# Performance work log

Measured on AMD Instinct MI355X. Metric: run time of the kernel, lower is better.

The kernel has to match this reference:

```python
import jax, jax.numpy as jnp
import numpy as np

B, L, HID, NH, HD = 2, 2048, 512, 8, 64
FACTOR = 5
SAMPLE_K = 40  # min(factor * ceil(ln(L)), L)
N_TOP = 40     # min(factor * ceil(ln(L)), L)


def setup_inputs() -> dict:
    key = jax.random.key(0)
    ks = jax.random.split(key, 10)
    s = 1.0 / np.sqrt(HID).astype(np.float32)
    return {
        "hidden_states": jax.random.normal(ks[0], (B, L, HID), jnp.float32),
        "index_sample": jax.random.randint(ks[1], (L, SAMPLE_K), 0, L, jnp.int32),
        "Wq": jax.random.normal(ks[2], (HID, HID), jnp.float32) * s,
        "bq": jnp.zeros((HID,), jnp.float32),
        "Wk": jax.random.normal(ks[3], (HID, HID), jnp.float32) * s,
        "bk": jnp.zeros((HID,), jnp.float32),
        "Wv": jax.random.normal(ks[4], (HID, HID), jnp.float32) * s,
        "bv": jnp.zeros((HID,), jnp.float32),
        "Wo": jax.random.normal(ks[5], (HID, HID), jnp.float32) * s,
        "bo": jnp.zeros((HID,), jnp.float32),
    }


def _heads(x):
    # [B, L, HID] -> [B, NH, L, HD]
    return x.reshape(B, L, NH, HD).transpose(0, 2, 1, 3)


def reference(hidden_states, index_sample, Wq, bq, Wk, bk, Wv, bv, Wo, bo):
    # projections (torch Linear: x @ W.T + b)
    q = _heads(hidden_states @ Wq.T + bq)  # [B,NH,L,HD]
    k = _heads(hidden_states @ Wk.T + bk)
    v = _heads(hidden_states @ Wv.T + bv)

    # --- prob QK: random key sampling per query position ---
    # gather sampled keys: [B,NH,L,SAMPLE_K,HD]
    k_samp = k[:, :, index_sample, :]
    qk_samp = jnp.einsum('bhld,bhlsd->bhls', q, k_samp)
    # sparsity measure M(q) = max - mean (mean uses full k_len as in source)
    m = qk_samp.max(axis=-1) - qk_samp.sum(axis=-1) / L  # [B,NH,L]
    _, m_top = jax.lax.top_k(m, N_TOP)  # [B,NH,N_TOP]

    # selected queries -> dense scores against all keys
    q_red = jnp.take_along_axis(q, m_top[..., None], axis=2)  # [B,NH,N_TOP,HD]
    scores = jnp.einsum('bhqd,bhkd->bhqk', q_red, k) / np.sqrt(HD).astype(np.float32)

    # --- context: mean(V) baseline, scatter attended rows (no mask, eval dropout) ---
    attn = jax.nn.softmax(scores, axis=-1)  # [B,NH,N_TOP,L]
    ctx_sel = jnp.einsum('bhqk,bhkd->bhqd', attn, v)  # [B,NH,N_TOP,HD]
    context = jnp.broadcast_to(v.mean(axis=2, keepdims=True), (B, NH, L, HD))
    bi = jnp.arange(B)[:, None, None]
    hi = jnp.arange(NH)[None, :, None]
    context = context.at[bi, hi, m_top].set(ctx_sel)  # [B,NH,L,HD]

    out = context.transpose(0, 2, 1, 3).reshape(B, L, HID) @ Wo.T + bo
    return out
```

## Files before the change

### kernel.cpp

```cpp
#include <hip/hip_runtime.h>
#include <hip/hip_bf16.h>
#include <math.h>

#define B_   2
#define L_   2048
#define HID_ 512
#define NH_  8
#define HD_  64
#define SK_  40
#define NTOP_ 40
#define NBH_ (B_ * NH_)
#define NROW_ (B_ * L_)
#define CHUNK_ 64
#define NCH_ (L_ / CHUNK_)
#define NTILE_ 64

__global__ __launch_bounds__(256, 2) void proj_kernel(
    const float* __restrict__ A,
    const float* __restrict__ Wq, const float* __restrict__ bq,
    const float* __restrict__ Wk, const float* __restrict__ bk,
    const float* __restrict__ Wv, const float* __restrict__ bv,
    float* __restrict__ qo, float* __restrict__ ko, float* __restrict__ vo,
    float* __restrict__ vmp)
{
    __shared__ __align__(16) float As[32][68];
    __shared__ __align__(16) float Bs[3][32][68];
    __shared__ float red[16][64];

    const float* Ws[3]  = {Wq, Wk, Wv};
    const float* bs3[3] = {bq, bk, bv};
    float*       os3[3] = {qo, ko, vo};

    const int t    = threadIdx.x;
    const int row0 = blockIdx.x * 64;
    const int h    = blockIdx.y;
    const int col0 = h * 64;
    const int ry   = t >> 4;
    const int cx   = t & 15;
    const int a_k4 = t & 7;
    const int sub  = t >> 3;

    float acc[3][4][4] = {};
    float4 pa[2], pb[3][2];

    #pragma unroll
    for (int i = 0; i < 2; ++i)
        pa[i] = *reinterpret_cast<const float4*>(
            &A[(size_t)(row0 + i * 32 + sub) * HID_ + (a_k4 << 2)]);
    #pragma unroll
    for (int w = 0; w < 3; ++w)
        #pragma unroll
        for (int i = 0; i < 2; ++i)
            pb[w][i] = *reinterpret_cast<const float4*>(
                &Ws[w][(size_t)(col0 + i * 32 + sub) * HID_ + (a_k4 << 2)]);

    for (int ks = 0; ks < 16; ++ks) {
        #pragma unroll
        for (int i = 0; i < 2; ++i) {
            const int a_row = i * 32 + sub;
            const int slot = (a_row >> 2) ^ a_k4;
            float* p = &As[a_k4 << 2][slot * 4 + (a_row & 3)];
            p[0 * 68] = pa[i].x; p[1 * 68] = pa[i].y;
            p[2 * 68] = pa[i].z; p[3 * 68] = pa[i].w;
        }
        #pragma unroll
        for (int w = 0; w < 3; ++w)
            #pragma unroll
            for (int i = 0; i < 2; ++i) {
                const int b_col = i * 32 + sub;
                const int slot = (b_col >> 2) ^ a_k4;
                float* p = &Bs[w][a_k4 << 2][slot * 4 + (b_col & 3)];
                p[0 * 68] = pb[w][i].x; p[1 * 68] = pb[w][i].y;
                p[2 * 68] = pb[w][i].z; p[3 * 68] = pb[w][i].w;
            }
        __syncthreads();

        if (ks < 15) {
            const int k0 = (ks + 1) * 32;
            #pragma unroll
            for (int i = 0; i < 2; ++i)
                pa[i] = *reinterpret_cast<const float4*>(
                    &A[(size_t)(row0 + i * 32 + sub) * HID_ + k0 + (a_k4 << 2)]);
            #pragma unroll
            for (int w = 0; w < 3; ++w)
                #pragma unroll
                for (int i = 0; i < 2; ++i)
                    pb[w][i] = *reinterpret_cast<const float4*>(
                        &Ws[w][(size_t)(col0 + i * 32 + sub) * HID_ + k0 + (a_k4 << 2)]);
        }

        #pragma unroll
        for (int kk = 0; kk < 32; ++kk) {
            const int v = kk >> 2;
            const float4 a0 = *reinterpret_cast<const float4*>(
                &As[kk][(ry ^ v) << 2]);
            const float as[4] = {a0.x, a0.y, a0.z, a0.w};
            #pragma unroll
            for (int w = 0; w < 3; ++w) {
                const float4 b0 = *reinterpret_cast<const float4*>(
                    &Bs[w][kk][(cx ^ v) << 2]);
                #pragma unroll
                for (int i = 0; i < 4; ++i) {
                    acc[w][i][0] = fmaf(as[i], b0.x, acc[w][i][0]);
                    acc[w][i][1] = fmaf(as[i], b0.y, acc[w][i][1]);
                    acc[w][i][2] = fmaf(as[i], b0.z, acc[w][i][2]);
                    acc[w][i][3] = fmaf(as[i], b0.w, acc[w][i][3]);
                }
            }
        }
        __syncthreads();
    }

    const int b_ = row0 >> 11;
    float4 bbv;
    #pragma unroll
    for (int w = 0; w < 3; ++w) {
        const float4 bb = *reinterpret_cast<const float4*>(&bs3[w][col0 + (cx << 2)]);
        if (w == 2) bbv = bb;
        #pragma unroll
        for (int i = 0; i < 4; ++i) {
            const int row = row0 + ry * 4 + i;
            const int l   = row & (L_ - 1);
            float4 ob;
            ob.x = acc[w][i][0] + bb.x;
            ob.y = acc[w][i][1] + bb.y;
            ob.z = acc[w][i][2] + bb.z;
            ob.w = acc[w][i][3] + bb.w;
            *reinterpret_cast<float4*>(
                &os3[w][(((size_t)(b_ * NH_ + h)) * L_ + l) * HD_ + (cx << 2)]) = ob;
        }
    }

    #pragma unroll
    for (int j = 0; j < 4; ++j) {
        float s_ = 0.f;
        #pragma unroll
        for (int i = 0; i < 4; ++i) s_ += acc[2][i][j];
        const float bj = (j == 0) ? bbv.x : (j == 1) ? bbv.y : (j == 2) ? bbv.z : bbv.w;
        red[ry][(cx << 2) + j] = s_ + 4.f * bj;
    }
    __syncthreads();
    if (t < 64) {
        float s_ = 0.f;
        #pragma unroll
        for (int r = 0; r < 16; ++r) s_ += red[r][t];
        vmp[((size_t)blockIdx.x * NH_ + h) * HD_ + t] = s_;
    }
}

__global__ __launch_bounds__(512) void base_kernel(
    const float* __restrict__ vmp, const float* __restrict__ Wo,
    const float* __restrict__ bo, float* __restrict__ vmean,
    float* __restrict__ base_out)
{
    const int b = blockIdx.x;
    const int t = threadIdx.x;
    __shared__ float vm[HID_];

    float s = 0.f;
    #pragma unroll
    for (int tl = 0; tl < 32; ++tl)
        s += vmp[((size_t)(b * 32 + tl) * NH_) * HD_ + t];
    const float mv = s * (1.0f / (float)L_);
    vmean[b * HID_ + t] = mv;
    vm[t] = mv;
    __syncthreads();

    float acc = bo[t];
    for (int c = 0; c < HID_; c += 4) {
        float4 w = *reinterpret_cast<const float4*>(&Wo[(size_t)t * HID_ + c]);
        acc = fmaf(vm[c + 0], w.x, acc);
        acc = fmaf(vm[c + 1], w.y, acc);
        acc = fmaf(vm[c + 2], w.z, acc);
        acc = fmaf(vm[c + 3], w.w, acc);
    }
    base_out[b * HID_ + t] = acc;
}

__global__ __launch_bounds__(256) void sample_m_kernel(
    const float* __restrict__ q, const float* __restrict__ k,
    const int* __restrict__ idx, float* __restrict__ m)
{
    const int wid  = blockIdx.x * 4 + (threadIdx.x >> 6);
    const int lane = threadIdx.x & 63;
    const int bh = wid >> 11;
    const int l  = wid & (L_ - 1);
    const int grp = lane >> 4, gl = lane & 15;

    const float4 qf = *reinterpret_cast<const float4*>(&q[(bh * L_ + l) * HD_ + (gl << 2)]);

    float mx = -INFINITY, sm = 0.f;
    #pragma unroll
    for (int it = 0; it < 10; ++it) {
        const int s  = it * 4 + grp;
        const int ki = idx[l * SK_ + s];
        const float4 kf = *reinterpret_cast<const float4*>(&k[(bh * L_ + ki) * HD_ + (gl << 2)]);
        float p = qf.x * kf.x + qf.y * kf.y + qf.z * kf.z + qf.w * kf.w;
        p += __shfl_xor(p, 1);
        p += __shfl_xor(p, 2);
        p += __shfl_xor(p, 4);
        p += __shfl_xor(p, 8);
        mx = fmaxf(mx, p);
        sm += p;
    }
    mx = fmaxf(mx, __shfl_xor(mx, 16));
    mx = fmaxf(mx, __shfl_xor(mx, 32));
    sm += __shfl_xor(sm, 16);
    sm += __shfl_xor(sm, 32);
    if (lane == 0) m[bh * L_ + l] = mx - sm * (1.0f / (float)L_);
}

__global__ __launch_bounds__(256) void topk_kernel(
    const float* __restrict__ m, int* __restrict__ m_top)
{
    const int bh = blockIdx.x;
    const int t  = threadIdx.x;
    const int lane = t & 63, wv = t >> 6;

    unsigned xv[8];
    #pragma unroll
    for (int i = 0; i < 8; ++i) {
        unsigned x = __float_as_uint(m[bh * L_ + i * 256 + t]);
        xv[i] = (x & 0x80000000u) ? ~x : (x | 0x80000000u);
    }

    __shared__ int cnt[2][4];
    __shared__ int s_outcnt, s_tieCnt;
    __shared__ int tie[256];
    if (t == 0) { s_outcnt = 0; s_tieCnt = 0; }

    unsigned pref = 0;
    for (int bit = 31; bit >= 0; --bit) {
        const unsigned test = pref | (1u << bit);
        int c = 0;
        #pragma unroll
        for (int i = 0; i < 8; ++i) c += (xv[i] >= test);
        #pragma unroll
        for (int off = 1; off < 64; off <<= 1) c += __shfl_xor(c, off);
        if (lane == 0) cnt[bit & 1][wv] = c;
        __syncthreads();
        const int tot = cnt[bit & 1][0] + cnt[bit & 1][1]
                      + cnt[bit & 1][2] + cnt[bit & 1][3];
        if (tot >= NTOP_) pref = test;
    }
    const unsigned V = pref;

    #pragma unroll
    for (int i = 0; i < 8; ++i) {
        const unsigned x = xv[i];
        const int idxv = i * 256 + t;
        if (x > V) {
            const int p = atomicAdd(&s_outcnt, 1);
            m_top[bh * NTOP_ + p] = idxv;
        } else if (x == V) {
            const int p = atomicAdd(&s_tieCnt, 1);
            if (p < 256) tie[p] = idxv;
        }
    }
    __syncthreads();
    if (t == 0) {
        const int rem = NTOP_ - s_outcnt;
        int n = s_tieCnt; if (n > 256) n = 256;
        for (int r = 0; r < rem; ++r) {
            int best = 1 << 30, bj = -1;
            for (int j2 = 0; j2 < n; ++j2)
                if (tie[j2] < best) { best = tie[j2]; bj = j2; }
            tie[bj] = 1 << 30;
            m_top[bh * NTOP_ + s_outcnt + r] = best;
        }
    }
}

__global__ __launch_bounds__(256) void attn_part_kernel(
    const float* __restrict__ q, const float* __restrict__ k,
    const float* __restrict__ v, const int* __restrict__ m_top,
    float* __restrict__ mx_p, float* __restrict__ sm_p, float* __restrict__ ctx_p)
{
    const int chunk = blockIdx.x;
    const int bh    = blockIdx.y;
    const int t = threadIdx.x;

    __shared__ __align__(16) float  Qs[NTOP_][64];
    __shared__ float4 Ks4[CHUNK_ * 16];
    __shared__ __align__(16) float  Vs[CHUNK_][64];
    __shared__ float  S[NTOP_][CHUNK_];

    for (int i = t; i < NTOP_ * 16; i += 256) {
        int qi = i >> 4, cc = i & 15;
        int l = m_top[bh * NTOP_ + qi];
        *reinterpret_cast<float4*>(&Qs[qi][cc << 2]) =
            *reinterpret_cast<const float4*>(&q[(bh * L_ + l) * HD_ + (cc << 2)]);
    }
    const int base = (bh * L_ + chunk * CHUNK_) * HD_;
    for (int i = t; i < CHUNK_ * 16; i += 256) {
        int r = i >> 4, cc = i & 15;
        Ks4[r * 16 + (cc ^ (r & 7))] =
            *reinterpret_cast<const float4*>(&k[base + r * HD_ + (cc << 2)]);
        *reinterpret_cast<float4*>(&Vs[r][cc << 2]) =
            *reinterpret_cast<const float4*>(&v[base + r * HD_ + (cc << 2)]);
    }
    __syncthreads();

    for (int o = t; o < NTOP_ * CHUNK_; o += 256) {
        int qi = o >> 6, j = o & (CHUNK_ - 1);
        float acc = 0.f;
        #pragma unroll
        for (int cc = 0; cc < 16; ++cc) {
            float4 kf = Ks4[j * 16 + (cc ^ (j & 7))];
            float4 qf = *reinterpret_cast<const float4*>(&Qs[qi][cc << 2]);
            acc = fmaf(qf.x, kf.x, acc);
            acc = fmaf(qf.y, kf.y, acc);
            acc = fmaf(qf.z, kf.z, acc);
            acc = fmaf(qf.w, kf.w, acc);
        }
        S[qi][j] = acc * 0.125f;
    }
    __syncthreads();

    const int gl = t & 31;
    for (int qi = t >> 5; qi < NTOP_; qi += 8) {
        float v0 = S[qi][gl], v1 = S[qi][gl + 32];
        float mx = fmaxf(v0, v1);
        #pragma unroll
        for (int off = 1; off < 32; off <<= 1) mx = fmaxf(mx, __shfl_xor(mx, off));
        float e0 = __expf(v0 - mx), e1 = __expf(v1 - mx);
        float sm = e0 + e1;
        #pragma unroll
        for (int off = 1; off < 32; off <<= 1) sm += __shfl_xor(sm, off);
        S[qi][gl] = e0; S[qi][gl + 32] = e1;
        if (gl == 0) {
            mx_p[(bh * NCH_ + chunk) * NTOP_ + qi] = mx;
            sm_p[(bh * NCH_ + chunk) * NTOP_ + qi] = sm;
        }
    }
    __syncthreads();

    for (int o = t; o < NTOP_ * HD_; o += 256) {
        int qi = o >> 6, d = o & 63;
        float acc = 0.f;
        #pragma unroll 8
        for (int j = 0; j < CHUNK_; ++j) acc = fmaf(S[qi][j], Vs[j][d], acc);
        ctx_p[((bh * NCH_ + chunk) * NTOP_ + qi) * HD_ + d] = acc;
    }
}

__global__ __launch_bounds__(256) void fill_kernel(
    const float* __restrict__ base_out, float* __restrict__ out)
{
    const int i = blockIdx.x * 256 + threadIdx.x;
    if (i >= NROW_ * (HID_ / 4)) return;
    const int j4  = i & 127;
    const int row = i >> 7;
    const int b   = row >> 11;
    reinterpret_cast<float4*>(out)[i] =
        reinterpret_cast<const float4*>(base_out)[b * 128 + j4];
}

__global__ __launch_bounds__(256) void combscat_kernel(
    const float* __restrict__ mx_p, const float* __restrict__ sm_p,
    const float* __restrict__ ctx_p, const float* __restrict__ vmean,
    const int* __restrict__ m_top, const float* __restrict__ Wo,
    float* __restrict__ out)
{
    const int bq = blockIdx.x;
    const int bh = bq / NTOP_, qi = bq % NTOP_;
    const int b = bh >> 3, h = bh & 7;
    const int t = threadIdx.x;
    const int g = t >> 6, d = t & 63;

    __shared__ float Mg[4], Dg[4];
    __shared__ float Ag[4][64];
    __shared__ float delta[64];

    float mxs[8];
    #pragma unroll
    for (int c8 = 0; c8 < 8; ++c8)
        mxs[c8] = mx_p[(bh * NCH_ + g * 8 + c8) * NTOP_ + qi];
    float M = mxs[0];
    #pragma unroll
    for (int c8 = 1; c8 < 8; ++c8) M = fmaxf(M, mxs[c8]);
    float den = 0.f, acc = 0.f;
    #pragma unroll
    for (int c8 = 0; c8 < 8; ++c8) {
        const int c = g * 8 + c8;
        const float w = __expf(mxs[c8] - M);
        den = fmaf(sm_p[(bh * NCH_ + c) * NTOP_ + qi], w, den);
        acc = fmaf(ctx_p[((bh * NCH_ + c) * NTOP_ + qi) * HD_ + d], w, acc);
    }
    if (d == 0) { Mg[g] = M; Dg[g] = den; }
    Ag[g][d] = acc;
    __syncthreads();
    if (t < 64) {
        const float MM = fmaxf(fmaxf(Mg[0], Mg[1]), fmaxf(Mg[2], Mg[3]));
        float dd = 0.f, aa = 0.f;
        #pragma unroll
        for (int gg = 0; gg < 4; ++gg) {
            const float w = __expf(Mg[gg] - MM);
            dd = fmaf(Dg[gg], w, dd);
            aa = fmaf(Ag[gg][t], w, aa);
        }
        delta[t] = aa / dd - vmean[bh * HD_ + t];
    }
    __syncthreads();
    const int l = m_top[bh * NTOP_ + qi];
    for (int j = t; j < HID_; j += 256) {
        float a2 = 0.f;
        #pragma unroll
        for (int c = 0; c < HD_; c += 4) {
            float4 w = *reinterpret_cast<const float4*>(&Wo[(size_t)j * HID_ + h * HD_ + c]);
            a2 = fmaf(delta[c + 0], w.x, a2);
            a2 = fmaf(delta[c + 1], w.y, a2);
            a2 = fmaf(delta[c + 2], w.z, a2);
            a2 = fmaf(delta[c + 3], w.w, a2);
        }
        atomicAdd(&out[((size_t)(b * L_ + l)) * HID_ + j], a2);
    }
}

extern "C" void kernel_launch(void* const* d_in, const int* in_sizes, int n_in,
                              void* d_out, int out_size, void* d_ws, size_t ws_size,
                              hipStream_t stream)
{
    const float* hs  = (const float*)d_in[0];
    const int*   idx = (const int*)  d_in[1];
    const float* Wq  = (const float*)d_in[2];
    const float* bq  = (const float*)d_in[3];
    const float* Wk  = (const float*)d_in[4];
    const float* bk  = (const float*)d_in[5];
    const float* Wv  = (const float*)d_in[6];
    const float* bv  = (const float*)d_in[7];
    const float* Wo  = (const float*)d_in[8];
    const float* bo  = (const float*)d_in[9];
    float* out = (float*)d_out;

    float* ws = (float*)d_ws;
    const size_t OFF_Q      = 0;
    const size_t OFF_K      = OFF_Q + (size_t)NBH_ * L_ * HD_;
    const size_t OFF_V      = OFF_K + (size_t)NBH_ * L_ * HD_;
    const size_t OFF_M      = OFF_V + (size_t)NBH_ * L_ * HD_;
    const size_t OFF_VMP    = OFF_M + (size_t)NBH_ * L_;
    const size_t OFF_VMEAN  = OFF_VMP + (size_t)NTILE_ * NH_ * HD_;
    const size_t OFF_MXP    = OFF_VMEAN + (size_t)NBH_ * HD_;
    const size_t OFF_SMP    = OFF_MXP + (size_t)NBH_ * NCH_ * NTOP_;
    const size_t OFF_CTXP   = OFF_SMP + (size_t)NBH_ * NCH_ * NTOP_;
    const size_t OFF_BASE   = OFF_CTXP + (size_t)NBH_ * NCH_ * NTOP_ * HD_;
    const size_t OFF_TOP    = OFF_BASE + (size_t)B_ * HID_;

    float* q_      = ws + OFF_Q;
    float* k_      = ws + OFF_K;
    float* v_      = ws + OFF_V;
    float* m_      = ws + OFF_M;
    float* vmp_    = ws + OFF_VMP;
    float* vmean_  = ws + OFF_VMEAN;
    float* mxp_    = ws + OFF_MXP;
    float* smp_    = ws + OFF_SMP;
    float* ctxp_   = ws + OFF_CTXP;
    float* base_   = ws + OFF_BASE;
    int*   mtop_   = (int*)(ws + OFF_TOP);

    proj_kernel<<<dim3(NROW_ / 64, NH_), 256, 0, stream>>>(
        hs, Wq, bq, Wk, bk, Wv, bv, q_, k_, v_, vmp_);
    base_kernel<<<B_, 512, 0, stream>>>(vmp_, Wo, bo, vmean_, base_);
    sample_m_kernel<<<(NBH_ * L_) / 4, 256, 0, stream>>>(q_, k_, idx, m_);
    topk_kernel<<<NBH_, 256, 0, stream>>>(m_, mtop_);
    attn_part_kernel<<<dim3(NCH_, NBH_), 256, 0, stream>>>(
        q_, k_, v_, mtop_, mxp_, smp_, ctxp_);
    fill_kernel<<<(NROW_ * (HID_ / 4) + 255) / 256, 256, 0, stream>>>(base_, out);
    combscat_kernel<<<NBH_ * NTOP_, 256, 0, stream>>>(
        mxp_, smp_, ctxp_, vmean_, mtop_, Wo, out);
}
```

Before: 258.1 us.

## Fuse base and fill kernels into sample and attention kernels; vectorise PV

The mean-V and base-output projection now runs in the first two blocks of sample_m_kernel. The broadcast fill of the output runs at the start of attn_part_kernel. This removes two kernel launches and their dependency gaps. The PV accumulation now processes four head dims per thread using float4 shared loads. The trade-off is that the base computation adds serial work to two blocks of sample_m.

Result: faster. 234.3 us (-9.2%).

```diff
diff --git a/kernel.cpp b/kernel.cpp
--- a/kernel.cpp
+++ b/kernel.cpp
@@ -148,41 +148,47 @@
     }
 }
 
-__global__ __launch_bounds__(512) void base_kernel(
+__global__ __launch_bounds__(256) void sample_m_kernel(
+    const float* __restrict__ q, const float* __restrict__ k,
+    const int* __restrict__ idx, float* __restrict__ m,
     const float* __restrict__ vmp, const float* __restrict__ Wo,
     const float* __restrict__ bo, float* __restrict__ vmean,
     float* __restrict__ base_out)
 {
-    const int b = blockIdx.x;
+    __shared__ float vm[HID_];
     const int t = threadIdx.x;
-    __shared__ float vm[HID_];
-
-    float s = 0.f;
-    #pragma unroll
-    for (int tl = 0; tl < 32; ++tl)
-        s += vmp[((size_t)(b * 32 + tl) * NH_) * HD_ + t];
-    const float mv = s * (1.0f / (float)L_);
-    vmean[b * HID_ + t] = mv;
-    vm[t] = mv;
-    __syncthreads();
-
-    float acc = bo[t];
-    for (int c = 0; c < HID_; c += 4) {
-        float4 w = *reinterpret_cast<const float4*>(&Wo[(size_t)t * HID_ + c]);
-        acc = fmaf(vm[c + 0], w.x, acc);
-        acc = fmaf(vm[c + 1], w.y, acc);
-        acc = fmaf(vm[c + 2], w.z, acc);
-        acc = fmaf(vm[c + 3], w.w, acc);
-    }
-    base_out[b * HID_ + t] = acc;
-}
-
-__global__ __launch_bounds__(256) void sample_m_kernel(
-    const float* __restrict__ q, const float* __restrict__ k,
-    const int* __restrict__ idx, float* __restrict__ m)
-{
-    const int wid  = blockIdx.x * 4 + (threadIdx.x >> 6);
-    const int lane = threadIdx.x & 63;
+
+    if (blockIdx.x < B_) {
+        const int b = blockIdx.x;
+        #pragma unroll
+        for (int jj = 0; jj < 2; ++jj) {
+            const int j = t + jj * 256;
+            float s = 0.f;
+            #pragma unroll
+            for (int tl = 0; tl < 32; ++tl)
+                s += vmp[(size_t)(b * 32 + tl) * HID_ + j];
+            const float mv = s * (1.0f / (float)L_);
+            vmean[b * HID_ + j] = mv;
+            vm[j] = mv;
+        }
+        __syncthreads();
+        #pragma unroll
+        for (int jj = 0; jj < 2; ++jj) {
+            const int j = t + jj * 256;
+            float acc = bo[j];
+            for (int c = 0; c < HID_; c += 4) {
+                float4 w = *reinterpret_cast<const float4*>(&Wo[(size_t)j * HID_ + c]);
+                acc = fmaf(vm[c + 0], w.x, acc);
+                acc = fmaf(vm[c + 1], w.y, acc);
+                acc = fmaf(vm[c + 2], w.z, acc);
+                acc = fmaf(vm[c + 3], w.w, acc);
+            }
+            base_out[b * HID_ + j] = acc;
+        }
+    }
+
+    const int wid  = blockIdx.x * 4 + (t >> 6);
+    const int lane = t & 63;
     const int bh = wid >> 11;
     const int l  = wid & (L_ - 1);
     const int grp = lane >> 4, gl = lane & 15;
@@ -274,11 +280,25 @@
 __global__ __launch_bounds__(256) void attn_part_kernel(
     const float* __restrict__ q, const float* __restrict__ k,
     const float* __restrict__ v, const int* __restrict__ m_top,
+    const float* __restrict__ base_out, float* __restrict__ out,
     float* __restrict__ mx_p, float* __restrict__ sm_p, float* __restrict__ ctx_p)
 {
     const int chunk = blockIdx.x;
     const int bh    = blockIdx.y;
     const int t = threadIdx.x;
+
+    {
+        const int f = bh * NCH_ + chunk;
+        const float4* b4 = reinterpret_cast<const float4*>(base_out);
+        float4* o4 = reinterpret_cast<float4*>(out);
+        #pragma unroll
+        for (int k2 = 0; k2 < 4; ++k2) {
+            const int i = f * 1024 + k2 * 256 + t;
+            const int j4 = i & 127;
+            const int b  = i >> 18;
+            o4[i] = b4[b * 128 + j4];
+        }
+    }
 
     __shared__ __align__(16) float  Qs[NTOP_][64];
     __shared__ float4 Ks4[CHUNK_ * 16];
@@ -335,25 +355,21 @@
     }
     __syncthreads();
 
-    for (int o = t; o < NTOP_ * HD_; o += 256) {
-        int qi = o >> 6, d = o & 63;
-        float acc = 0.f;
+    for (int o = t; o < NTOP_ * 16; o += 256) {
+        const int qi = o >> 4, d4 = (o & 15) << 2;
+        float4 a4 = {0.f, 0.f, 0.f, 0.f};
         #pragma unroll 8
-        for (int j = 0; j < CHUNK_; ++j) acc = fmaf(S[qi][j], Vs[j][d], acc);
-        ctx_p[((bh * NCH_ + chunk) * NTOP_ + qi) * HD_ + d] = acc;
-    }
-}
-
-__global__ __launch_bounds__(256) void fill_kernel(
-    const float* __restrict__ base_out, float* __restrict__ out)
-{
-    const int i = blockIdx.x * 256 + threadIdx.x;
-    if (i >= NROW_ * (HID_ / 4)) return;
-    const int j4  = i & 127;
-    const int row = i >> 7;
-    const int b   = row >> 11;
-    reinterpret_cast<float4*>(out)[i] =
-        reinterpret_cast<const float4*>(base_out)[b * 128 + j4];
+        for (int j = 0; j < CHUNK_; ++j) {
+            const float s = S[qi][j];
+            const float4 v4 = *reinterpret_cast<const float4*>(&Vs[j][d4]);
+            a4.x = fmaf(s, v4.x, a4.x);
+            a4.y = fmaf(s, v4.y, a4.y);
+            a4.z = fmaf(s, v4.z, a4.z);
+            a4.w = fmaf(s, v4.w, a4.w);
+        }
+        *reinterpret_cast<float4*>(
+            &ctx_p[((size_t)(bh * NCH_ + chunk) * NTOP_ + qi) * HD_ + d4]) = a4;
+    }
 }
 
 __global__ __launch_bounds__(256) void combscat_kernel(
@@ -385,7 +401,7 @@
         const int c = g * 8 + c8;
         const float w = __expf(mxs[c8] - M);
         den = fmaf(sm_p[(bh * NCH_ + c) * NTOP_ + qi], w, den);
-        acc = fmaf(ctx_p[((bh * NCH_ + c) * NTOP_ + qi) * HD_ + d], w, acc);
+        acc = fmaf(ctx_p[((size_t)(bh * NCH_ + c) * NTOP_ + qi) * HD_ + d], w, acc);
     }
     if (d == 0) { Mg[g] = M; Dg[g] = den; }
     Ag[g][d] = acc;
@@ -460,12 +476,11 @@
 
     proj_kernel<<<dim3(NROW_ / 64, NH_), 256, 0, stream>>>(
         hs, Wq, bq, Wk, bk, Wv, bv, q_, k_, v_, vmp_);
-    base_kernel<<<B_, 512, 0, stream>>>(vmp_, Wo, bo, vmean_, base_);
-    sample_m_kernel<<<(NBH_ * L_) / 4, 256, 0, stream>>>(q_, k_, idx, m_);
+    sample_m_kernel<<<(NBH_ * L_) / 4, 256, 0, stream>>>(
+        q_, k_, idx, m_, vmp_, Wo, bo, vmean_, base_);
     topk_kernel<<<NBH_, 256, 0, stream>>>(m_, mtop_);
     attn_part_kernel<<<dim3(NCH_, NBH_), 256, 0, stream>>>(
-        q_, k_, v_, mtop_, mxp_, smp_, ctxp_);
-    fill_kernel<<<(NROW_ * (HID_ / 4) + 255) / 256, 256, 0, stream>>>(base_, out);
+        q_, k_, v_, mtop_, base_, out, mxp_, smp_, ctxp_);
     combscat_kernel<<<NBH_ * NTOP_, 256, 0, stream>>>(
         mxp_, smp_, ctxp_, vmean_, mtop_, Wo, out);
 }
```
